# Kernel optimization log

Measured on AMD Instinct MI355X. Metric: run time of the kernel, lower is better.

## Reference

```python
import jax, jax.numpy as jnp
import numpy as np

K = 8192
D = 512
BETA = 0.25


def setup_inputs() -> dict:
    key = jax.random.key(0)
    k_z, k_cb = jax.random.split(key)
    z = jax.random.normal(k_z, (8, 4096, D), dtype=jnp.float32)
    codebook = jax.random.normal(k_cb, (K, D), dtype=jnp.float32)
    return {"z": z, "codebook": codebook}


def reference(z, codebook):
    B, Q, Din = z.shape
    flat = z.reshape(-1, Din)                      # (N, D)
    x2 = jnp.sum(flat * flat, axis=1, keepdims=True)   # (N, 1)
    e2 = jnp.sum(codebook * codebook, axis=1)          # (K,)
    xe = flat @ codebook.T                             # (N, K)
    distances = x2 - 2.0 * xe + e2[None, :]
    indices = jnp.argmin(distances, axis=1)            # (N,)
    z_q = codebook[indices].reshape(B, Q, Din)

    codebook_loss = jnp.mean((z_q - jax.lax.stop_gradient(z)) ** 2)
    commitment_loss = jnp.mean((z - jax.lax.stop_gradient(z_q)) ** 2)
    vq_loss = codebook_loss + BETA * commitment_loss
    z_q_ste = z + jax.lax.stop_gradient(z_q - z)

    # perplexity from one-hot usage counts of this batch
    N = flat.shape[0]
    counts = jnp.zeros((codebook.shape[0],), dtype=jnp.float32).at[indices].add(1.0)
    probs = counts / jnp.asarray(N, dtype=jnp.float32)
    perplexity = jnp.exp(-jnp.sum(probs * jnp.log(probs + 1e-10)))

    return z_q_ste, vq_loss, indices.reshape(B, Q), perplexity
```

## Files before the change

kernel.cpp:

```cpp
#include <hip/hip_runtime.h>
#include <hip/hip_bf16.h>

#define K_CODES 8192
#define DIM     512
#define N_VEC   32768
#define MARGIN  0.5f

typedef __attribute__((ext_vector_type(8))) short   short8;
typedef __attribute__((ext_vector_type(8))) unsigned short ushort8;
typedef __attribute__((ext_vector_type(4))) float   float4x;

__device__ inline void gl_lds16(const void* g, void* l) {
    __builtin_amdgcn_global_load_lds(
        (const __attribute__((address_space(1))) unsigned int*)g,
        (__attribute__((address_space(3))) unsigned int*)l, 16, 0, 0);
}

__device__ inline unsigned short f2bf(float f) {
    unsigned int u = __float_as_uint(f);
    return (unsigned short)((u + 0x7FFFu + ((u >> 16) & 1u)) >> 16);
}

__device__ inline float med3(float a, float b, float c) {
    return __builtin_amdgcn_fmed3f(a, b, c);
}

__global__ __launch_bounds__(256) void vq_prep(
    const float* __restrict__ z, const float* __restrict__ cb,
    float* __restrict__ x2, float* __restrict__ hne2,
    unsigned short* __restrict__ zh, unsigned short* __restrict__ ch) {
    int wave = threadIdx.x >> 6;
    int lane = threadIdx.x & 63;
    int row  = blockIdx.x * 4 + wave;
    bool isZ = row < N_VEC;
    int lr = isZ ? row : row - N_VEC;
    const float* src = isZ ? z + (size_t)row * DIM : cb + (size_t)lr * DIM;

    const float4* s4 = (const float4*)src;
    float4 v0 = s4[lane * 2];
    float4 v1 = s4[lane * 2 + 1];
    float f[8] = {v0.x, v0.y, v0.z, v0.w, v1.x, v1.y, v1.z, v1.w};

    float s = 0.0f;
    ushort8 h8;
#pragma unroll
    for (int i = 0; i < 8; ++i) { s += f[i] * f[i]; h8[i] = f2bf(f[i]); }
    ((ushort8*)(isZ ? zh : ch))[(size_t)lr * 64 + lane] = h8;

#pragma unroll
    for (int off = 32; off >= 1; off >>= 1) s += __shfl_xor(s, off, 64);
    if (lane == 0) {
        if (isZ) x2[lr] = s;
        else     hne2[lr] = -0.5f * s;
    }
}

__global__ __launch_bounds__(256, 2) void vq_gemm(
    const unsigned short* __restrict__ zh, const unsigned short* __restrict__ ch,
    const float* __restrict__ hne2,
    float* __restrict__ pG, int* __restrict__ pN, float* __restrict__ pG2,
    int* __restrict__ pN2, float* __restrict__ pG3) {
    __shared__ short8 AsC[1024];
    __shared__ short8 BsC[2048];

    const int tid  = threadIdx.x;
    const int w    = tid >> 6;
    const int lane = tid & 63;
    const int wM   = w & 1;
    const int wN   = w >> 1;
    const int rowBase   = blockIdx.x * 128;
    const int half      = blockIdx.y;
    const int codeBase0 = half * 4096;

    const int low3 = lane & 7, m15 = lane & 15, hi4 = lane >> 4;

    unsigned aOff[4];
#pragma unroll
    for (int i = 0; i < 4; ++i) {
        int cell = (w * 4 + i) * 64 + lane;
        int r = cell >> 3, qs = cell & 7, q = qs ^ (r & 7);
        aOff[i] = ((unsigned)(rowBase + r) * DIM + q * 8) * 2;
    }
    unsigned bOff[8];
#pragma unroll
    for (int i = 0; i < 8; ++i) {
        int cell = (w * 8 + i) * 64 + lane;
        int c = cell >> 3, qs = cell & 7, q = qs ^ (c & 7);
        bOff[i] = ((unsigned)c * DIM + q * 8) * 2;
    }

    int rIdx[4], cIdx[8];
#pragma unroll
    for (int mf = 0; mf < 4; ++mf) rIdx[mf] = (wM * 64 + mf * 16 + m15) * 8;
#pragma unroll
    for (int nf = 0; nf < 8; ++nf) cIdx[nf] = (wN * 128 + nf * 16 + m15) * 8;

    float g1v[4][4], g2v[4][4], g3v[4][4];
#pragma unroll
    for (int mf = 0; mf < 4; ++mf)
#pragma unroll
        for (int rg = 0; rg < 4; ++rg) {
            g1v[mf][rg] = -3.4e38f; g2v[mf][rg] = -3.4e38f; g3v[mf][rg] = -3.4e38f;
        }

    const char* pA = (const char*)zh;
    for (int ct = 0; ct < 16; ++ct) {
        const int codeBase = codeBase0 + ct * 256;
        const char* pB = (const char*)ch + (size_t)codeBase * (DIM * 2);
        float4x acc[4][8];
#pragma unroll
        for (int mf = 0; mf < 4; ++mf)
#pragma unroll
            for (int nf = 0; nf < 8; ++nf) acc[mf][nf] = (float4x){0.f, 0.f, 0.f, 0.f};

        for (int dc = 0; dc < DIM; dc += 64) {
            const int dc2 = dc * 2;
            __syncthreads();
#pragma unroll
            for (int i = 0; i < 4; ++i)
                gl_lds16(pA + aOff[i] + dc2, &AsC[(w * 4 + i) * 64]);
#pragma unroll
            for (int i = 0; i < 8; ++i)
                gl_lds16(pB + bOff[i] + dc2, &BsC[(w * 8 + i) * 64]);
            __syncthreads();

#pragma unroll
            for (int ks = 0; ks < 2; ++ks) {
                const int qx = (ks * 4 + hi4) ^ low3;
                short8 a[4];
#pragma unroll
                for (int mf = 0; mf < 4; ++mf) a[mf] = AsC[rIdx[mf] + qx];
#pragma unroll
                for (int nf = 0; nf < 8; ++nf) {
                    short8 b = BsC[cIdx[nf] + qx];
#pragma unroll
                    for (int mf = 0; mf < 4; ++mf)
                        acc[mf][nf] = __builtin_amdgcn_mfma_f32_16x16x32_bf16(
                            a[mf], b, acc[mf][nf], 0, 0, 0);
                }
            }
        }

#pragma unroll
        for (int nf = 0; nf < 8; ++nf) {
            int nb = codeBase + wN * 128 + nf * 16 + m15;
            float hv = hne2[nb];
            unsigned tag = ((unsigned)ct << 7) | ((unsigned)nf << 4) | (unsigned)m15;
#pragma unroll
            for (int mf = 0; mf < 4; ++mf) {
#pragma unroll
                for (int rg = 0; rg < 4; ++rg) {
                    float g  = acc[mf][nf][rg] + hv;
                    float pk = __uint_as_float(
                        (__float_as_uint(g) & 0xFFFFF800u) | tag);
                    g3v[mf][rg] = med3(pk, g2v[mf][rg], g3v[mf][rg]);
                    g2v[mf][rg] = med3(pk, g1v[mf][rg], g2v[mf][rg]);
                    g1v[mf][rg] = fmaxf(g1v[mf][rg], pk);
                }
            }
        }
    }

#pragma unroll
    for (int mf = 0; mf < 4; ++mf)
#pragma unroll
        for (int rg = 0; rg < 4; ++rg) {
            float a1 = g1v[mf][rg], a2 = g2v[mf][rg], a3 = g3v[mf][rg];
#pragma unroll
            for (int off = 1; off <= 8; off <<= 1) {
                float b1 = __shfl_xor(a1, off, 64);
                float b2 = __shfl_xor(a2, off, 64);
                float b3 = __shfl_xor(a3, off, 64);
                a3 = med3(b1, a2, a3);
                a2 = med3(b1, a1, a2);
                a1 = fmaxf(a1, b1);
                a3 = med3(b2, a2, a3);
                a2 = med3(b2, a1, a2);
                a3 = med3(b3, a2, a3);
            }
            if (m15 == 0) {
                unsigned u1 = __float_as_uint(a1);
                unsigned u2 = __float_as_uint(a2);
                unsigned u3 = __float_as_uint(a3);
                int t1 = (int)(u1 & 0x7FFu), t2 = (int)(u2 & 0x7FFu);
                int c1 = codeBase0 + ((t1 & 0x780) << 1) + wN * 128 + (t1 & 0x7F);
                int c2 = codeBase0 + ((t2 & 0x780) << 1) + wN * 128 + (t2 & 0x7F);
                int row  = rowBase + wM * 64 + mf * 16 + hi4 * 4 + rg;
                int slot = half * 2 + wN;
                pG [slot * N_VEC + row] = __uint_as_float(u1 & 0xFFFFF800u);
                pN [slot * N_VEC + row] = c1;
                pG2[slot * N_VEC + row] = __uint_as_float(u2 & 0xFFFFF800u);
                pN2[slot * N_VEC + row] = c2;
                pG3[slot * N_VEC + row] = __uint_as_float(u3 & 0xFFFFF800u);
            }
        }
}

__global__ __launch_bounds__(256) void vq_scan(
    float* __restrict__ pG, const int* __restrict__ pN,
    const float* __restrict__ pG2, const int* __restrict__ pN2,
    const float* __restrict__ pG3,
    int* __restrict__ provIdx, int* __restrict__ flags,
    unsigned long long* __restrict__ keys,
    int* __restrict__ rescueRows, int* __restrict__ rescueCnt,
    int* __restrict__ pairRows, int* __restrict__ pairCnt,
    int* __restrict__ mergedN2) {
    int r = blockIdx.x * 256 + threadIdx.x;
    float g1 = pG[r], g2 = pG2[r], g3 = pG3[r];
    int   n1 = pN[r], n2 = pN2[r];
#pragma unroll
    for (int s = 1; s < 4; ++s) {
        float a1 = pG [s * N_VEC + r];
        int  an1 = pN [s * N_VEC + r];
        float a2 = pG2[s * N_VEC + r];
        int  an2 = pN2[s * N_VEC + r];
        float a3 = pG3[s * N_VEC + r];
        if (a1 > g1 || (a1 == g1 && an1 < n1)) {
            g3 = g2; g2 = g1; n2 = n1; g1 = a1; n1 = an1;
        } else if (a1 > g2 || (a1 == g2 && an1 < n2)) {
            g3 = g2; g2 = a1; n2 = an1;
        } else g3 = fmaxf(g3, a1);
        if (a2 > g1 || (a2 == g1 && an2 < n1)) {
            g3 = g2; g2 = g1; n2 = n1; g1 = a2; n1 = an2;
        } else if (a2 > g2 || (a2 == g2 && an2 < n2)) {
            g3 = g2; g2 = a2; n2 = an2;
        } else g3 = fmaxf(g3, a2);
        g3 = fmaxf(g3, a3);
    }
    provIdx[r] = n1;
    pG[r] = g1;
    int fl = 0;
    if (g1 - g3 < MARGIN) {
        fl = 1; keys[r] = ~0ull;
        int p = atomicAdd(rescueCnt, 1);
        rescueRows[p] = r;
    } else if (g1 - g2 < MARGIN) {
        fl = 1; keys[r] = ~0ull;
        mergedN2[r] = n2;
        int p = atomicAdd(pairCnt, 1);
        pairRows[p] = r;
    }
    flags[r] = fl;
}

__global__ __launch_bounds__(256) void vq_pair(
    const float* __restrict__ z, const float* __restrict__ cb,
    const float* __restrict__ hne2,
    const int* __restrict__ provIdx, const int* __restrict__ mergedN2,
    const int* __restrict__ pairRows, const int* __restrict__ pairCnt,
    unsigned long long* __restrict__ keys) {
    const int lane = threadIdx.x & 63;
    const int wid  = blockIdx.x * 4 + (threadIdx.x >> 6);
    const int nW   = gridDim.x * 4;
    const int cnt  = *pairCnt;
    for (int i = wid; i < cnt; i += nW) {
        int r  = pairRows[i];
        int n1 = provIdx[r];
        int n2 = mergedN2[r];
        const float4* xz = (const float4*)(z  + (size_t)r  * DIM);
        const float4* c1 = (const float4*)(cb + (size_t)n1 * DIM);
        const float4* c2 = (const float4*)(cb + (size_t)n2 * DIM);
        float4 x0 = xz[lane * 2], x1 = xz[lane * 2 + 1];
        float4 a0 = c1[lane * 2], a1 = c1[lane * 2 + 1];
        float4 b0 = c2[lane * 2], b1 = c2[lane * 2 + 1];
        float d1 = x0.x*a0.x + x0.y*a0.y + x0.z*a0.z + x0.w*a0.w
                 + x1.x*a1.x + x1.y*a1.y + x1.z*a1.z + x1.w*a1.w;
        float d2 = x0.x*b0.x + x0.y*b0.y + x0.z*b0.z + x0.w*b0.w
                 + x1.x*b1.x + x1.y*b1.y + x1.z*b1.z + x1.w*b1.w;
#pragma unroll
        for (int off = 32; off >= 1; off >>= 1) {
            d1 += __shfl_xor(d1, off, 64);
            d2 += __shfl_xor(d2, off, 64);
        }
        if (lane == 0) {
            float kv1 = -hne2[n1] - d1;
            float kv2 = -hne2[n2] - d2;
            int nsel; float kv;
            if (kv2 < kv1 || (kv2 == kv1 && n2 < n1)) { kv = kv2; nsel = n2; }
            else                                      { kv = kv1; nsel = n1; }
            keys[r] = ((unsigned long long)__float_as_uint(kv) << 32) |
                      (unsigned long long)(unsigned)nsel;
        }
    }
}

#define RBM 64
#define RBK 256
#define RBD 32

__global__ __launch_bounds__(256, 2) void vq_rescue(
    const float* __restrict__ z, const float* __restrict__ cb,
    const float* __restrict__ hne2,
    const int* __restrict__ rescueRows, const int* __restrict__ rescueCnt,
    unsigned long long* __restrict__ keys) {
    __shared__ float As[RBD][RBM];
    __shared__ float Bs[RBD][RBK];
    __shared__ int   rowOf[RBM];

    const int tid = threadIdx.x;
    const int tx  = tid & 31;
    const int ty  = tid >> 5;
    const int cnt = *rescueCnt;
    const int codeBase = blockIdx.y * RBK;
    const int sRow = tid >> 2;
    const int sQ   = tid & 3;

    for (int rt = blockIdx.x; rt * RBM < cnt; rt += gridDim.x) {
        const int slotBase = rt * RBM;
        __syncthreads();
        if (tid < RBM) rowOf[tid] = rescueRows[slotBase + tid];
        __syncthreads();

        float acc[8][8];
#pragma unroll
        for (int i = 0; i < 8; ++i)
#pragma unroll
            for (int j = 0; j < 8; ++j) acc[i][j] = 0.0f;

        for (int dc = 0; dc < DIM; dc += RBD) {
            __syncthreads();
            {
                const float* srcA = z + (size_t)rowOf[sRow] * DIM + dc + sQ * 8;
                float4 va0 = ((const float4*)srcA)[0];
                float4 va1 = ((const float4*)srcA)[1];
                int c0 = sQ * 8;
                As[c0 + 0][sRow] = va0.x; As[c0 + 1][sRow] = va0.y;
                As[c0 + 2][sRow] = va0.z; As[c0 + 3][sRow] = va0.w;
                As[c0 + 4][sRow] = va1.x; As[c0 + 5][sRow] = va1.y;
                As[c0 + 6][sRow] = va1.z; As[c0 + 7][sRow] = va1.w;
            }
            {
                const float4* srcB = (const float4*)(cb + (size_t)(codeBase + tid) * DIM + dc);
#pragma unroll
                for (int j = 0; j < 8; ++j) {
                    float4 v = srcB[j];
                    Bs[j * 4 + 0][tid] = v.x; Bs[j * 4 + 1][tid] = v.y;
                    Bs[j * 4 + 2][tid] = v.z; Bs[j * 4 + 3][tid] = v.w;
                }
            }
            __syncthreads();

#pragma unroll
            for (int d = 0; d < RBD; ++d) {
                float a[8], b[8];
                *(float4*)&a[0] = *(const float4*)&As[d][ty * 8];
                *(float4*)&a[4] = *(const float4*)&As[d][ty * 8 + 4];
#pragma unroll
                for (int j = 0; j < 8; ++j) b[j] = Bs[d][tx + 32 * j];
#pragma unroll
                for (int i = 0; i < 8; ++i)
#pragma unroll
                    for (int j = 0; j < 8; ++j) acc[i][j] += a[i] * b[j];
            }
        }

        float best[8];
        int   bidx[8];
#pragma unroll
        for (int i = 0; i < 8; ++i) { best[i] = 3.4e38f; bidx[i] = K_CODES; }

#pragma unroll
        for (int j = 0; j < 8; ++j) {
            int code = codeBase + tx + 32 * j;
            float ev = -hne2[code];
#pragma unroll
            for (int i = 0; i < 8; ++i) {
                float kv = ev - acc[i][j];
                if (kv < best[i] || (kv == best[i] && code < bidx[i])) {
                    best[i] = kv;
                    bidx[i] = code;
                }
            }
        }

#pragma unroll
        for (int off = 16; off >= 1; off >>= 1) {
#pragma unroll
            for (int i = 0; i < 8; ++i) {
                float od = __shfl_xor(best[i], off, 64);
                int   oi = __shfl_xor(bidx[i], off, 64);
                if (od < best[i] || (od == best[i] && oi < bidx[i])) {
                    best[i] = od;
                    bidx[i] = oi;
                }
            }
        }

        if (tx == 0) {
#pragma unroll
            for (int i = 0; i < 8; ++i) {
                int slot = slotBase + ty * 8 + i;
                if (slot < cnt) {
                    unsigned long long key =
                        ((unsigned long long)__float_as_uint(best[i]) << 32) |
                        (unsigned long long)(unsigned)bidx[i];
                    atomicMin(&keys[rowOf[ty * 8 + i]], key);
                }
            }
        }
    }
}

__global__ __launch_bounds__(256) void vq_final(
    const float* __restrict__ gBest, const int* __restrict__ provIdx,
    const int* __restrict__ flags, const unsigned long long* __restrict__ keys,
    const float* __restrict__ x2, const float* __restrict__ cb,
    float* __restrict__ zq, float* __restrict__ idxf,
    float* __restrict__ counts, float* __restrict__ lossAcc) {
    __shared__ int   sIdx[256];
    __shared__ float wsum[4];
    const int tid = threadIdx.x;
    const int r   = blockIdx.x * 256 + tid;

    int n; float dist;
    if (flags[r]) {
        unsigned long long k = keys[r];
        n = (int)(unsigned)(k & 0xffffffffu);
        float kv = __uint_as_float((unsigned)(k >> 32));
        dist = x2[r] + 2.0f * kv;
    } else {
        n = provIdx[r];
        dist = x2[r] - 2.0f * gBest[r];
    }
    sIdx[tid] = n;
    idxf[r]   = (float)n;
    atomicAdd(&counts[n], 1.0f);

    float ls = dist;
#pragma unroll
    for (int off = 32; off >= 1; off >>= 1) ls += __shfl_xor(ls, off, 64);
    if ((tid & 63) == 0) wsum[tid >> 6] = ls;
    __syncthreads();
    if (tid == 0) atomicAdd(lossAcc, wsum[0] + wsum[1] + wsum[2] + wsum[3]);

    const float4* cb4 = (const float4*)cb;
    float4* zq4 = (float4*)(zq + (size_t)blockIdx.x * 256 * DIM);
    for (int t = tid; t < 256 * (DIM / 4); t += 256) {
        int row = t >> 7, f4 = t & 127;
        zq4[(size_t)row * 128 + f4] = cb4[(size_t)sIdx[row] * 128 + f4];
    }
}

__global__ __launch_bounds__(256) void vq_finalize(const float* __restrict__ counts,
                                                   const float* __restrict__ lossAcc,
                                                   float* __restrict__ out_loss,
                                                   float* __restrict__ out_perp) {
    __shared__ float wsum[4];
    int tid = threadIdx.x;
    float s = 0.0f;
    for (int i = tid; i < K_CODES; i += 256) {
        float p = counts[i] * (1.0f / (float)N_VEC);
        s += p * logf(p + 1e-10f);
    }
#pragma unroll
    for (int off = 32; off >= 1; off >>= 1) s += __shfl_xor(s, off, 64);
    if ((tid & 63) == 0) wsum[tid >> 6] = s;
    __syncthreads();
    if (tid == 0) {
        *out_perp = expf(-(wsum[0] + wsum[1] + wsum[2] + wsum[3]));
        *out_loss = 1.25f * lossAcc[0] / (float)(N_VEC * DIM);
    }
}

extern "C" void kernel_launch(void* const* d_in, const int* in_sizes, int n_in,
                              void* d_out, int out_size, void* d_ws, size_t ws_size,
                              hipStream_t stream) {
    (void)in_sizes; (void)n_in; (void)out_size; (void)ws_size;
    const float* z  = (const float*)d_in[0];
    const float* cb = (const float*)d_in[1];

    char* ws = (char*)d_ws;
    float* x2        = (float*)(ws + 0);
    float* hne2      = (float*)(ws + 131072);
    float* counts    = (float*)(ws + 163840);
    float* lossAcc   = (float*)(ws + 196608);
    int*   rescueCnt = (int*)  (ws + 196612);
    int*   pairCnt   = (int*)  (ws + 196616);
    int*   provIdx   = (int*)  (ws + 262144);
    int*   flags     = (int*)  (ws + 393216);
    unsigned long long* keys = (unsigned long long*)(ws + 524288);
    int*   rescueRows = (int*) (ws + 786432);
    float* pG        = (float*)(ws + 1048576);
    int*   pN        = (int*)  (ws + 1572864);
    float* pG2       = (float*)(ws + 2097152);
    unsigned short* zh = (unsigned short*)(ws + 2621440);
    unsigned short* ch = (unsigned short*)(ws + 36175872);

    float* out      = (float*)d_out;
    float* zq       = out;
    float* out_loss = out + 16777216;
    float* idxf     = out + 16777217;
    float* out_perp = out + 16777217 + 32768;

    char* sc = (char*)d_out;
    int*   pN2      = (int*)  (sc + 0);
    float* pG3      = (float*)(sc + 524288);
    int*   mergedN2 = (int*)  (sc + 1048576);
    int*   pairRows = (int*)  (sc + 1179648);

    hipMemsetAsync(counts, 0, 32768 + 16, stream);
    hipMemsetAsync(rescueRows, 0, 131072, stream);
    vq_prep<<<(N_VEC + K_CODES) / 4, 256, 0, stream>>>(z, cb, x2, hne2, zh, ch);
    dim3 grid(N_VEC / 128, 2);
    vq_gemm<<<grid, 256, 0, stream>>>(zh, ch, hne2, pG, pN, pG2, pN2, pG3);
    vq_scan<<<N_VEC / 256, 256, 0, stream>>>(pG, pN, pG2, pN2, pG3, provIdx, flags,
                                             keys, rescueRows, rescueCnt,
                                             pairRows, pairCnt, mergedN2);
    vq_pair<<<128, 256, 0, stream>>>(z, cb, hne2, provIdx, mergedN2,
                                     pairRows, pairCnt, keys);
    dim3 rgrid(32, 32);
    vq_rescue<<<rgrid, 256, 0, stream>>>(z, cb, hne2, rescueRows, rescueCnt, keys);
    vq_final<<<N_VEC / 256, 256, 0, stream>>>(pG, provIdx, flags, keys, x2, cb,
                                              zq, idxf, counts, lossAcc);
    vq_finalize<<<1, 256, 0, stream>>>(counts, lossAcc, out_loss, out_perp);
}
```

Before: 716.4 us.

## Restructure VQ GEMM into 256x256 tiles with double-buffered LDS and partial top-3 slots

The distance GEMM now gives each 512-thread block one 256-row by 256-code tile instead of looping over 16 code tiles per block. LDS is double-buffered so the next K-slice loads while MFMAs run, and MFMA sections are wrapped in raised wave priority. Each block writes packed top-3 candidates into 128 slots per row, and the scan kernel merges those instead of 4 slots. This trades the long serial code loop and its per-chunk syncs for more parallel blocks, at the cost of much larger partial-result traffic and a heavier scan. The tighter margin and smaller rescue grid also shrink the fallback work.

```diff
diff --git a/kernel.cpp b/kernel.cpp
--- a/kernel.cpp
+++ b/kernel.cpp
@@ -4,7 +4,7 @@
 #define K_CODES 8192
 #define DIM     512
 #define N_VEC   32768
-#define MARGIN  0.5f
+#define MARGIN  0.4f
 
 typedef __attribute__((ext_vector_type(8))) short   short8;
 typedef __attribute__((ext_vector_type(8))) unsigned short ushort8;
@@ -55,117 +55,121 @@
     }
 }
 
-__global__ __launch_bounds__(256, 2) void vq_gemm(
+__global__ __launch_bounds__(512, 2) void vq_gemm(
     const unsigned short* __restrict__ zh, const unsigned short* __restrict__ ch,
     const float* __restrict__ hne2,
-    float* __restrict__ pG, int* __restrict__ pN, float* __restrict__ pG2,
-    int* __restrict__ pN2, float* __restrict__ pG3) {
-    __shared__ short8 AsC[1024];
-    __shared__ short8 BsC[2048];
+    float* __restrict__ pP1, float* __restrict__ pP2, float* __restrict__ pP3) {
+    __shared__ short8 As[2][2048];
+    __shared__ short8 Bs[2][2048];
 
     const int tid  = threadIdx.x;
     const int w    = tid >> 6;
     const int lane = tid & 63;
-    const int wM   = w & 1;
-    const int wN   = w >> 1;
-    const int rowBase   = blockIdx.x * 128;
-    const int half      = blockIdx.y;
-    const int codeBase0 = half * 4096;
+    const int wM   = w >> 2;
+    const int wN   = w & 3;
+    const int rowBase  = blockIdx.x * 256;
+    const int codeBase = blockIdx.y * 256;
 
     const int low3 = lane & 7, m15 = lane & 15, hi4 = lane >> 4;
 
-    unsigned aOff[4];
+    unsigned aOff[4], bOff[4];
 #pragma unroll
     for (int i = 0; i < 4; ++i) {
         int cell = (w * 4 + i) * 64 + lane;
         int r = cell >> 3, qs = cell & 7, q = qs ^ (r & 7);
-        aOff[i] = ((unsigned)(rowBase + r) * DIM + q * 8) * 2;
-    }
-    unsigned bOff[8];
-#pragma unroll
-    for (int i = 0; i < 8; ++i) {
-        int cell = (w * 8 + i) * 64 + lane;
-        int c = cell >> 3, qs = cell & 7, q = qs ^ (c & 7);
-        bOff[i] = ((unsigned)c * DIM + q * 8) * 2;
-    }
-
-    int rIdx[4], cIdx[8];
-#pragma unroll
-    for (int mf = 0; mf < 4; ++mf) rIdx[mf] = (wM * 64 + mf * 16 + m15) * 8;
-#pragma unroll
-    for (int nf = 0; nf < 8; ++nf) cIdx[nf] = (wN * 128 + nf * 16 + m15) * 8;
-
-    float g1v[4][4], g2v[4][4], g3v[4][4];
-#pragma unroll
-    for (int mf = 0; mf < 4; ++mf)
+        aOff[i] = ((unsigned)(rowBase  + r) * DIM + q * 8) * 2;
+        bOff[i] = ((unsigned)(codeBase + r) * DIM + q * 8) * 2;
+    }
+
+    int rIdx[8], cIdx[4];
+#pragma unroll
+    for (int mf = 0; mf < 8; ++mf) rIdx[mf] = (wM * 128 + mf * 16 + m15) * 8;
+#pragma unroll
+    for (int nf = 0; nf < 4; ++nf) cIdx[nf] = (wN * 64 + nf * 16 + m15) * 8;
+
+    float4x acc[8][4];
+#pragma unroll
+    for (int mf = 0; mf < 8; ++mf)
+#pragma unroll
+        for (int nf = 0; nf < 4; ++nf) acc[mf][nf] = (float4x){0.f, 0.f, 0.f, 0.f};
+
+    const char* pA = (const char*)zh;
+    const char* pB = (const char*)ch;
+
+#pragma unroll
+    for (int i = 0; i < 4; ++i) {
+        gl_lds16(pA + aOff[i], &As[0][(w * 4 + i) * 64]);
+        gl_lds16(pB + bOff[i], &Bs[0][(w * 4 + i) * 64]);
+    }
+    __syncthreads();
+
+    int cur = 0;
+    for (int t = 0; t < 8; ++t) {
+        if (t < 7) {
+            const int dc2 = (t + 1) * 128;
+#pragma unroll
+            for (int i = 0; i < 4; ++i) {
+                gl_lds16(pA + aOff[i] + dc2, &As[cur ^ 1][(w * 4 + i) * 64]);
+                gl_lds16(pB + bOff[i] + dc2, &Bs[cur ^ 1][(w * 4 + i) * 64]);
+            }
+        }
+#pragma unroll
+        for (int ks = 0; ks < 2; ++ks) {
+            const int qx = (ks * 4 + hi4) ^ low3;
+            short8 a[8];
+#pragma unroll
+            for (int mf = 0; mf < 8; ++mf) a[mf] = As[cur][rIdx[mf] + qx];
+            short8 b[4];
+#pragma unroll
+            for (int nf = 0; nf < 4; ++nf) b[nf] = Bs[cur][cIdx[nf] + qx];
+            __builtin_amdgcn_s_setprio(1);
+#pragma unroll
+            for (int nf = 0; nf < 4; ++nf)
+#pragma unroll
+                for (int mf = 0; mf < 8; ++mf)
+                    acc[mf][nf] = __builtin_amdgcn_mfma_f32_16x16x32_bf16(
+                        a[mf], b[nf], acc[mf][nf], 0, 0, 0);
+            __builtin_amdgcn_s_setprio(0);
+        }
+        __syncthreads();
+        cur ^= 1;
+    }
+
+    float hv[4];
+#pragma unroll
+    for (int nf = 0; nf < 4; ++nf)
+        hv[nf] = hne2[codeBase + wN * 64 + nf * 16 + m15];
+
+    float G1[8][4], G2[8][4], G3[8][4];
+#pragma unroll
+    for (int mf = 0; mf < 8; ++mf)
 #pragma unroll
         for (int rg = 0; rg < 4; ++rg) {
-            g1v[mf][rg] = -3.4e38f; g2v[mf][rg] = -3.4e38f; g3v[mf][rg] = -3.4e38f;
-        }
-
-    const char* pA = (const char*)zh;
-    for (int ct = 0; ct < 16; ++ct) {
-        const int codeBase = codeBase0 + ct * 256;
-        const char* pB = (const char*)ch + (size_t)codeBase * (DIM * 2);
-        float4x acc[4][8];
-#pragma unroll
-        for (int mf = 0; mf < 4; ++mf)
-#pragma unroll
-            for (int nf = 0; nf < 8; ++nf) acc[mf][nf] = (float4x){0.f, 0.f, 0.f, 0.f};
-
-        for (int dc = 0; dc < DIM; dc += 64) {
-            const int dc2 = dc * 2;
-            __syncthreads();
-#pragma unroll
-            for (int i = 0; i < 4; ++i)
-                gl_lds16(pA + aOff[i] + dc2, &AsC[(w * 4 + i) * 64]);
-#pragma unroll
-            for (int i = 0; i < 8; ++i)
-                gl_lds16(pB + bOff[i] + dc2, &BsC[(w * 8 + i) * 64]);
-            __syncthreads();
-
-#pragma unroll
-            for (int ks = 0; ks < 2; ++ks) {
-                const int qx = (ks * 4 + hi4) ^ low3;
-                short8 a[4];
-#pragma unroll
-                for (int mf = 0; mf < 4; ++mf) a[mf] = AsC[rIdx[mf] + qx];
-#pragma unroll
-                for (int nf = 0; nf < 8; ++nf) {
-                    short8 b = BsC[cIdx[nf] + qx];
-#pragma unroll
-                    for (int mf = 0; mf < 4; ++mf)
-                        acc[mf][nf] = __builtin_amdgcn_mfma_f32_16x16x32_bf16(
-                            a[mf], b, acc[mf][nf], 0, 0, 0);
-                }
-            }
-        }
-
-#pragma unroll
-        for (int nf = 0; nf < 8; ++nf) {
-            int nb = codeBase + wN * 128 + nf * 16 + m15;
-            float hv = hne2[nb];
-            unsigned tag = ((unsigned)ct << 7) | ((unsigned)nf << 4) | (unsigned)m15;
-#pragma unroll
-            for (int mf = 0; mf < 4; ++mf) {
-#pragma unroll
-                for (int rg = 0; rg < 4; ++rg) {
-                    float g  = acc[mf][nf][rg] + hv;
-                    float pk = __uint_as_float(
-                        (__float_as_uint(g) & 0xFFFFF800u) | tag);
-                    g3v[mf][rg] = med3(pk, g2v[mf][rg], g3v[mf][rg]);
-                    g2v[mf][rg] = med3(pk, g1v[mf][rg], g2v[mf][rg]);
-                    g1v[mf][rg] = fmaxf(g1v[mf][rg], pk);
-                }
-            }
-        }
-    }
-
-#pragma unroll
-    for (int mf = 0; mf < 4; ++mf)
+            G1[mf][rg] = -3.4e38f; G2[mf][rg] = -3.4e38f; G3[mf][rg] = -3.4e38f;
+        }
+
+#pragma unroll
+    for (int mf = 0; mf < 8; ++mf)
+#pragma unroll
+        for (int nf = 0; nf < 4; ++nf) {
+            unsigned tag = ((unsigned)nf << 4) | (unsigned)m15;
+#pragma unroll
+            for (int rg = 0; rg < 4; ++rg) {
+                float g  = acc[mf][nf][rg] + hv[nf];
+                float pk = __uint_as_float(
+                    (__float_as_uint(g) & 0xFFFFFFC0u) | tag);
+                G3[mf][rg] = med3(pk, G2[mf][rg], G3[mf][rg]);
+                G2[mf][rg] = med3(pk, G1[mf][rg], G2[mf][rg]);
+                G1[mf][rg] = fmaxf(G1[mf][rg], pk);
+            }
+        }
+
+    const int slot = blockIdx.y * 4 + wN;
+#pragma unroll
+    for (int mf = 0; mf < 8; ++mf)
 #pragma unroll
         for (int rg = 0; rg < 4; ++rg) {
-            float a1 = g1v[mf][rg], a2 = g2v[mf][rg], a3 = g3v[mf][rg];
+            float a1 = G1[mf][rg], a2 = G2[mf][rg], a3 = G3[mf][rg];
 #pragma unroll
             for (int off = 1; off <= 8; off <<= 1) {
                 float b1 = __shfl_xor(a1, off, 64);
@@ -179,56 +183,41 @@
                 a3 = med3(b3, a2, a3);
             }
             if (m15 == 0) {
-                unsigned u1 = __float_as_uint(a1);
-                unsigned u2 = __float_as_uint(a2);
-                unsigned u3 = __float_as_uint(a3);
-                int t1 = (int)(u1 & 0x7FFu), t2 = (int)(u2 & 0x7FFu);
-                int c1 = codeBase0 + ((t1 & 0x780) << 1) + wN * 128 + (t1 & 0x7F);
-                int c2 = codeBase0 + ((t2 & 0x780) << 1) + wN * 128 + (t2 & 0x7F);
-                int row  = rowBase + wM * 64 + mf * 16 + hi4 * 4 + rg;
-                int slot = half * 2 + wN;
-                pG [slot * N_VEC + row] = __uint_as_float(u1 & 0xFFFFF800u);
-                pN [slot * N_VEC + row] = c1;
-                pG2[slot * N_VEC + row] = __uint_as_float(u2 & 0xFFFFF800u);
-                pN2[slot * N_VEC + row] = c2;
-                pG3[slot * N_VEC + row] = __uint_as_float(u3 & 0xFFFFF800u);
+                int row = rowBase + wM * 128 + mf * 16 + hi4 * 4 + rg;
+                pP1[(size_t)slot * N_VEC + row] = a1;
+                pP2[(size_t)slot * N_VEC + row] = a2;
+                pP3[(size_t)slot * N_VEC + row] = a3;
             }
         }
 }
 
 __global__ __launch_bounds__(256) void vq_scan(
-    float* __restrict__ pG, const int* __restrict__ pN,
-    const float* __restrict__ pG2, const int* __restrict__ pN2,
-    const float* __restrict__ pG3,
-    int* __restrict__ provIdx, int* __restrict__ flags,
+    const float* __restrict__ pP1, const float* __restrict__ pP2,
+    const float* __restrict__ pP3,
+    float* __restrict__ pG, int* __restrict__ provIdx, int* __restrict__ flags,
     unsigned long long* __restrict__ keys,
     int* __restrict__ rescueRows, int* __restrict__ rescueCnt,
     int* __restrict__ pairRows, int* __restrict__ pairCnt,
     int* __restrict__ mergedN2) {
     int r = blockIdx.x * 256 + threadIdx.x;
-    float g1 = pG[r], g2 = pG2[r], g3 = pG3[r];
-    int   n1 = pN[r], n2 = pN2[r];
-#pragma unroll
-    for (int s = 1; s < 4; ++s) {
-        float a1 = pG [s * N_VEC + r];
-        int  an1 = pN [s * N_VEC + r];
-        float a2 = pG2[s * N_VEC + r];
-        int  an2 = pN2[s * N_VEC + r];
-        float a3 = pG3[s * N_VEC + r];
-        if (a1 > g1 || (a1 == g1 && an1 < n1)) {
-            g3 = g2; g2 = g1; n2 = n1; g1 = a1; n1 = an1;
-        } else if (a1 > g2 || (a1 == g2 && an1 < n2)) {
-            g3 = g2; g2 = a1; n2 = an1;
-        } else g3 = fmaxf(g3, a1);
-        if (a2 > g1 || (a2 == g1 && an2 < n1)) {
-            g3 = g2; g2 = g1; n2 = n1; g1 = a2; n1 = an2;
-        } else if (a2 > g2 || (a2 == g2 && an2 < n2)) {
-            g3 = g2; g2 = a2; n2 = an2;
-        } else g3 = fmaxf(g3, a2);
+    float g1 = -3.4e38f, g2 = -3.4e38f, g3 = -3.4e38f;
+    int   n1 = 0, n2 = 0;
+    for (int s = 0; s < 128; ++s) {
+        float a1 = pP1[(size_t)s * N_VEC + r];
+        float a2 = pP2[(size_t)s * N_VEC + r];
+        float a3 = pP3[(size_t)s * N_VEC + r];
+        int base = (s >> 2) * 256 + (s & 3) * 64;
+        int an1 = base + (int)(__float_as_uint(a1) & 0x3Fu);
+        int an2 = base + (int)(__float_as_uint(a2) & 0x3Fu);
+        if (a1 > g1)      { g3 = g2; g2 = g1; n2 = n1; g1 = a1; n1 = an1; }
+        else if (a1 > g2) { g3 = g2; g2 = a1; n2 = an1; }
+        else              g3 = fmaxf(g3, a1);
+        if (a2 > g2)      { g3 = g2; g2 = a2; n2 = an2; }
+        else              g3 = fmaxf(g3, a2);
         g3 = fmaxf(g3, a3);
     }
     provIdx[r] = n1;
-    pG[r] = g1;
+    pG[r] = __uint_as_float(__float_as_uint(g1) & 0xFFFFFFC0u);
     int fl = 0;
     if (g1 - g3 < MARGIN) {
         fl = 1; keys[r] = ~0ull;
@@ -481,8 +470,8 @@
     unsigned long long* keys = (unsigned long long*)(ws + 524288);
     int*   rescueRows = (int*) (ws + 786432);
     float* pG        = (float*)(ws + 1048576);
-    int*   pN        = (int*)  (ws + 1572864);
-    float* pG2       = (float*)(ws + 2097152);
+    int*   mergedN2  = (int*)  (ws + 1179648);
+    int*   pairRows  = (int*)  (ws + 1310720);
     unsigned short* zh = (unsigned short*)(ws + 2621440);
     unsigned short* ch = (unsigned short*)(ws + 36175872);
 
@@ -493,22 +482,21 @@
     float* out_perp = out + 16777217 + 32768;
 
     char* sc = (char*)d_out;
-    int*   pN2      = (int*)  (sc + 0);
-    float* pG3      = (float*)(sc + 524288);
-    int*   mergedN2 = (int*)  (sc + 1048576);
-    int*   pairRows = (int*)  (sc + 1179648);
+    float* pP1 = (float*)(sc + 0);
+    float* pP2 = (float*)(sc + 16777216);
+    float* pP3 = (float*)(sc + 33554432);
 
     hipMemsetAsync(counts, 0, 32768 + 16, stream);
     hipMemsetAsync(rescueRows, 0, 131072, stream);
     vq_prep<<<(N_VEC + K_CODES) / 4, 256, 0, stream>>>(z, cb, x2, hne2, zh, ch);
-    dim3 grid(N_VEC / 128, 2);
-    vq_gemm<<<grid, 256, 0, stream>>>(zh, ch, hne2, pG, pN, pG2, pN2, pG3);
-    vq_scan<<<N_VEC / 256, 256, 0, stream>>>(pG, pN, pG2, pN2, pG3, provIdx, flags,
+    dim3 grid(N_VEC / 256, K_CODES / 256);
+    vq_gemm<<<grid, 512, 0, stream>>>(zh, ch, hne2, pP1, pP2, pP3);
+    vq_scan<<<N_VEC / 256, 256, 0, stream>>>(pP1, pP2, pP3, pG, provIdx, flags,
                                              keys, rescueRows, rescueCnt,
                                              pairRows, pairCnt, mergedN2);
     vq_pair<<<128, 256, 0, stream>>>(z, cb, hne2, provIdx, mergedN2,
                                      pairRows, pairCnt, keys);
-    dim3 rgrid(32, 32);
+    dim3 rgrid(8, 32);
     vq_rescue<<<rgrid, 256, 0, stream>>>(z, cb, hne2, rescueRows, rescueCnt, keys);
     vq_final<<<N_VEC / 256, 256, 0, stream>>>(pG, provIdx, flags, keys, x2, cb,
                                               zq, idxf, counts, lossAcc);
```

After: 722.5 us. Within noise of the previous version (+0.9%).
